# Optimization experiments

Measured on AMD Instinct MI355X. Metric: run time of the kernel, lower is better.

The kernel has to match this reference:

```python
import jax, jax.numpy as jnp
import numpy as np

EMBED_DIM = 768
Q_DIM = 64
V_DIM = 64
WINDOW_SIZE = 3


def setup_inputs() -> dict:
    key = jax.random.key(0)
    ks = jax.random.split(key, 7)
    B, N = 4, 4096
    s = 1.0 / np.sqrt(EMBED_DIM)
    x = jax.random.normal(ks[0], (B, N, EMBED_DIM), dtype=jnp.float32)
    Wq = jax.random.normal(ks[1], (EMBED_DIM, Q_DIM), dtype=jnp.float32) * s
    bq = jax.random.normal(ks[2], (Q_DIM,), dtype=jnp.float32) * 0.01
    Wk = jax.random.normal(ks[3], (EMBED_DIM, Q_DIM), dtype=jnp.float32) * s
    bk = jax.random.normal(ks[4], (Q_DIM,), dtype=jnp.float32) * 0.01
    Wv = jax.random.normal(ks[5], (EMBED_DIM, V_DIM), dtype=jnp.float32) * s
    bv = jax.random.normal(ks[6], (V_DIM,), dtype=jnp.float32) * 0.01
    return {"x": x, "Wq": Wq, "bq": bq, "Wk": Wk, "bk": bk, "Wv": Wv, "bv": bv}


def reference(x, Wq, bq, Wk, bk, Wv, bv):
    # Faithful translation of SliddingWindowAttention.forward, including the
    # original's quirk: diagonal scores are written into columns 0..window_size-1
    # of a full (B, N, N) zero matrix, softmax is taken over ALL N columns
    # (zeros included), and the result is matmul'd with V.
    B, N, _ = x.shape
    Q = x @ Wq + bq  # (B, N, Q_DIM)
    K = x @ Wk + bk  # (B, N, Q_DIM)
    V = x @ Wv + bv  # (B, N, V_DIM)

    half = WINDOW_SIZE // 2
    columns = jnp.zeros((B, N, N), dtype=x.dtype)
    for idx, di in enumerate(range(-half, half + 1)):
        # diagonal offset di: pair row i with column j = i + di (valid rows only)
        rows = np.arange(max(0, -di), N - max(0, di))
        cols_j = rows + di
        c = jnp.einsum('bid,bid->bi', Q[:, rows, :], K[:, cols_j, :])
        columns = columns.at[:, rows, idx].set(c)

    attn = jax.nn.softmax(columns, axis=2)  # (B, N, N)
    return attn @ V  # (B, N, V_DIM)
```

## Files before the change

### kernel.cpp

```cpp
#include <hip/hip_runtime.h>
#include <hip/hip_bf16.h>
#include <math.h>

#define EMBED 768
#define NTOK  4096
#define NB    4
#define ROWS  16384
#define CN    192

typedef __attribute__((ext_vector_type(8))) short bf16x8;
typedef __attribute__((ext_vector_type(8))) unsigned short u16x8;
typedef __attribute__((ext_vector_type(4))) float f32x4;

struct hl16 { unsigned short h, l; };

__device__ inline hl16 split2(float f) {
  hl16 r;
  union { float f; unsigned u; } a; a.f = f;
  unsigned rr = (a.u + 0x7FFFu + ((a.u >> 16) & 1u)) & 0xFFFF0000u;
  r.h = (unsigned short)(rr >> 16);
  union { unsigned u; float f; } hf; hf.u = rr;
  union { float f; unsigned u; } b; b.f = f - hf.f;
  r.l = (unsigned short)((b.u + 0x7FFFu + ((b.u >> 16) & 1u)) >> 16);
  return r;
}

__device__ inline hl16 splitHW(float f) {
  hl16 r;
  __hip_bfloat16 hb = __float2bfloat16(f);
  float hf = __bfloat162float(hb);
  __hip_bfloat16 lb = __float2bfloat16(f - hf);
  r.h = __builtin_bit_cast(unsigned short, hb);
  r.l = __builtin_bit_cast(unsigned short, lb);
  return r;
}

__global__ __launch_bounds__(256) void prep(const float* __restrict__ x,
                                            const float* __restrict__ Wq,
                                            const float* __restrict__ Wk,
                                            const float* __restrict__ Wv,
                                            unsigned short* __restrict__ Wt,
                                            unsigned short* __restrict__ Xt,
                                            float* __restrict__ Vsum) {
  __shared__ float tile[32 * 64];
  const int bid = blockIdx.x;
  const int t   = threadIdx.x;

  if (bid < 6144) {
    const int u   = bid * 4 + (t >> 6);
    const int mt  = u / 24;
    const int ks  = u - mt * 24;
    const int lam = t & 63;
    const int ml  = lam & 15;
    const int q   = lam >> 4;
    const float* src = x + (size_t)(mt * 16 + ml) * EMBED + ks * 32 + q * 8;
    const float4 a0 = *(const float4*)src;
    const float4 a1 = *(const float4*)(src + 4);
    u16x8 hv, lv;
    hl16 s;
    s = splitHW(a0.x); hv[0] = s.h; lv[0] = s.l;
    s = splitHW(a0.y); hv[1] = s.h; lv[1] = s.l;
    s = splitHW(a0.z); hv[2] = s.h; lv[2] = s.l;
    s = splitHW(a0.w); hv[3] = s.h; lv[3] = s.l;
    s = splitHW(a1.x); hv[4] = s.h; lv[4] = s.l;
    s = splitHW(a1.y); hv[5] = s.h; lv[5] = s.l;
    s = splitHW(a1.z); hv[6] = s.h; lv[6] = s.l;
    s = splitHW(a1.w); hv[7] = s.h; lv[7] = s.l;
    unsigned short* dst = Xt + (size_t)(mt * 24 + ks) * 1024 + lam * 8;
    *(u16x8*)dst         = hv;
    *(u16x8*)(dst + 512) = lv;
    return;
  }

  const int b   = bid - 6144;
  const int mat = b / 24;
  const int ks  = b - mat * 24;
  const float* W = (mat == 0) ? Wq : (mat == 1) ? Wk : Wv;

  const float4* src = (const float4*)(W + ks * 2048);
  ((float4*)tile)[t]       = src[t];
  ((float4*)tile)[t + 256] = src[t + 256];
  __syncthreads();

  const int q    = t >> 6;
  const int nloc = t & 63;
  u16x8 hv, lv;
#pragma unroll
  for (int j = 0; j < 8; ++j) {
    hl16 s = split2(tile[(q * 8 + j) * 64 + nloc]);
    hv[j] = s.h; lv[j] = s.l;
  }

  const int n   = mat * 64 + nloc;
  const int nqb = n / 48;
  const int col = n - nqb * 48;
  unsigned short* dst = Wt + (size_t)nqb * 73728 + (size_t)ks * 3072 + q * 384 + col * 8;
  *(u16x8*)dst          = hv;
  *(u16x8*)(dst + 1536) = lv;

  if (b == 0) Vsum[t] = 0.f;
}

__device__ inline void gload_lds16(const unsigned short* g, unsigned short* l) {
  __builtin_amdgcn_global_load_lds(
      (const __attribute__((address_space(1))) unsigned int*)(g),
      (__attribute__((address_space(3))) unsigned int*)(l),
      16, 0, 0);
}

#define MF(A, B, ACC) ACC = __builtin_amdgcn_mfma_f32_16x16x32_bf16(A, B, ACC, 0, 0, 0)

__global__ __launch_bounds__(512, 2) void qkv_mfma(const unsigned short* __restrict__ Xt,
                                                   const unsigned short* __restrict__ Wtu,
                                                   const float* __restrict__ bq,
                                                   const float* __restrict__ bk,
                                                   const float* __restrict__ bv,
                                                   float* __restrict__ C,
                                                   float* __restrict__ Vsum) {
  extern __shared__ unsigned short lds[];

  const int tid  = threadIdx.x;
  const int lane = tid & 63;
  const int wm   = tid >> 6;
  const int nl   = lane & 15;
  const int q    = lane >> 4;
  const int bid  = blockIdx.x;
  const int mc   = (bid & 7) * 8 + (bid >> 5);
  const int nqb  = (bid >> 3) & 3;
  const int nbase = nqb * 48;
  const int r0w  = mc * 256 + wm * 32;
  const int mt0  = mc * 16 + wm * 2;

  {
    const unsigned short* g = Wtu + (size_t)nqb * 73728 + tid * 8;
    unsigned short* l = lds + tid * 8;
#pragma unroll
    for (int i = 0; i < 18; ++i)
      gload_lds16(g + i * 4096, l + i * 4096);
  }

  f32x4 acc00 = {0.f,0.f,0.f,0.f}, acc01 = {0.f,0.f,0.f,0.f}, acc02 = {0.f,0.f,0.f,0.f};
  f32x4 acc10 = {0.f,0.f,0.f,0.f}, acc11 = {0.f,0.f,0.f,0.f}, acc12 = {0.f,0.f,0.f,0.f};

  const bf16x8* XA0 = (const bf16x8*)Xt + (size_t)mt0 * 3072 + lane;
  const bf16x8* XA1 = XA0 + 3072;

  bf16x8 ah0 = XA0[0], al0 = XA0[64];
  bf16x8 ah1 = XA1[0], al1 = XA1[64];

  __syncthreads();

  const bf16x8* LB = (const bf16x8*)lds + q * 48 + nl;

  for (int ks = 0; ks < 24; ++ks) {
    const int o = ks * 384;
    bf16x8 bh0 = LB[o],       bh1 = LB[o + 16],  bh2 = LB[o + 32];
    bf16x8 bl0 = LB[o + 192], bl1 = LB[o + 208], bl2 = LB[o + 224];
    bf16x8 nh0, nl0, nh1, nl1;
    if (ks < 23) {
      nh0 = XA0[(ks + 1) * 128]; nl0 = XA0[(ks + 1) * 128 + 64];
      nh1 = XA1[(ks + 1) * 128]; nl1 = XA1[(ks + 1) * 128 + 64];
    }
    MF(ah0, bh0, acc00); MF(ah1, bh0, acc10);
    MF(ah0, bh1, acc01); MF(ah1, bh1, acc11);
    MF(ah0, bh2, acc02); MF(ah1, bh2, acc12);
    MF(ah0, bl0, acc00); MF(ah1, bl0, acc10);
    MF(ah0, bl1, acc01); MF(ah1, bl1, acc11);
    MF(ah0, bl2, acc02); MF(ah1, bl2, acc12);
    MF(al0, bh0, acc00); MF(al1, bh0, acc10);
    MF(al0, bh1, acc01); MF(al1, bh1, acc11);
    MF(al0, bh2, acc02); MF(al1, bh2, acc12);
    ah0 = nh0; al0 = nl0; ah1 = nh1; al1 = nl1;
  }

#define EPI(MI, NT, ACC) do {                                               \
    const int col = nbase + (NT) * 16 + nl;                                 \
    const float bias = (col < 64) ? bq[col]                                 \
                     : (col < 128) ? bk[col - 64] : bv[col - 128];          \
    const int row = r0w + (MI) * 16 + q * 4;                                \
    C[(size_t)(row + 0) * CN + col] = ACC[0] + bias;                        \
    C[(size_t)(row + 1) * CN + col] = ACC[1] + bias;                        \
    C[(size_t)(row + 2) * CN + col] = ACC[2] + bias;                        \
    C[(size_t)(row + 3) * CN + col] = ACC[3] + bias;                        \
  } while (0)

  EPI(0, 0, acc00); EPI(0, 1, acc01); EPI(0, 2, acc02);
  EPI(1, 0, acc10); EPI(1, 1, acc11); EPI(1, 2, acc12);

#define VS(NT, A0, A1) do {                                                 \
    const int col = nbase + (NT) * 16 + nl;                                 \
    if (col >= 128) {                                                       \
      float s = A0[0] + A0[1] + A0[2] + A0[3]                               \
              + A1[0] + A1[1] + A1[2] + A1[3] + 8.f * bv[col - 128];        \
      s += __shfl_xor(s, 16, 64);                                           \
      s += __shfl_xor(s, 32, 64);                                           \
      if (q == 0) atomicAdd(&Vsum[(r0w >> 12) * 64 + (col - 128)], s);      \
    }                                                                       \
  } while (0)

  VS(0, acc00, acc10); VS(1, acc01, acc11); VS(2, acc02, acc12);
}

__global__ __launch_bounds__(256) void attn_kernel(const float* __restrict__ C,
                                                   const float* __restrict__ Vsum,
                                                   float* __restrict__ out) {
  const int t    = threadIdx.x;
  const int lane = t & 63;
  const int wave = t >> 6;
  const int r = blockIdx.x * 4 + wave;
  const int b = r >> 12;
  const int i = r & (NTOK - 1);

  const float q  = C[(size_t)r * CN + lane];
  const float kc = C[(size_t)r * CN + 64 + lane];
  float km = 0.f, kp = 0.f;
  if (i > 0)        km = C[(size_t)(r - 1) * CN + 64 + lane];
  if (i < NTOK - 1) kp = C[(size_t)(r + 1) * CN + 64 + lane];

  float p0 = q * km, p1 = q * kc, p2 = q * kp;
#pragma unroll
  for (int off = 32; off > 0; off >>= 1) {
    p0 += __shfl_xor(p0, off, 64);
    p1 += __shfl_xor(p1, off, 64);
    p2 += __shfl_xor(p2, off, 64);
  }

  const float s0 = (i > 0) ? p0 : 0.f;
  const float s1 = p1;
  const float s2 = (i < NTOK - 1) ? p2 : 0.f;
  const float m  = fmaxf(fmaxf(s0, s1), fmaxf(s2, 0.f));
  const float e0 = expf(s0 - m);
  const float e1 = expf(s1 - m);
  const float e2 = expf(s2 - m);
  const float ez = expf(-m);
  const float Z  = e0 + e1 + e2 + (float)(NTOK - 3) * ez;

  const size_t vb = ((size_t)b * NTOK) * CN + 128;
  const float v0 = C[vb + lane];
  const float v1 = C[vb + CN + lane];
  const float v2 = C[vb + 2 * (size_t)CN + lane];
  const float vs = Vsum[b * 64 + lane];

  out[(size_t)r * 64 + lane] =
      (e0 * v0 + e1 * v1 + e2 * v2 + ez * (vs - v0 - v1 - v2)) / Z;
}

extern "C" void kernel_launch(void* const* d_in, const int* in_sizes, int n_in,
                              void* d_out, int out_size, void* d_ws, size_t ws_size,
                              hipStream_t stream) {
  const float* x  = (const float*)d_in[0];
  const float* Wq = (const float*)d_in[1];
  const float* bq = (const float*)d_in[2];
  const float* Wk = (const float*)d_in[3];
  const float* bk = (const float*)d_in[4];
  const float* Wv = (const float*)d_in[5];
  const float* bv = (const float*)d_in[6];
  float* out = (float*)d_out;

  float* C    = (float*)d_ws;
  float* Vsum = C + (size_t)ROWS * CN;
  unsigned short* Wt = (unsigned short*)(Vsum + NB * 64);
  unsigned short* Xt = Wt + 4 * 73728;

  prep<<<6216, 256, 0, stream>>>(x, Wq, Wk, Wv, Wt, Xt, Vsum);
  qkv_mfma<<<256, 512, 147456, stream>>>(Xt, Wt, bq, bk, bv, C, Vsum);
  attn_kernel<<<ROWS / 4, 256, 0, stream>>>(C, Vsum, out);
}
```

Before: 127.5 us.

## Split K dimension across two wave groups in QKV MFMA kernel with LDS reduction

Doubles the QKV GEMM block to 1024 threads and splits the 24-step K loop between two groups of eight waves, each handling half of K. The upper group writes its partial accumulators to LDS, which is reused after a barrier, and the lower group adds them before the bias epilogue and the V-sum atomics. This raises the number of waves per block to hide memory latency, since the grid has only 256 blocks. The cost is an extra LDS round trip and two barriers, plus higher register pressure under the 1024-thread launch bound.

Measured after the change: 127.5 us (median of 2 runs). About the same (-0.0%).

```diff
diff --git a/kernel.cpp b/kernel.cpp
--- a/kernel.cpp
+++ b/kernel.cpp
@@ -110,18 +110,20 @@
 
 #define MF(A, B, ACC) ACC = __builtin_amdgcn_mfma_f32_16x16x32_bf16(A, B, ACC, 0, 0, 0)
 
-__global__ __launch_bounds__(512, 2) void qkv_mfma(const unsigned short* __restrict__ Xt,
-                                                   const unsigned short* __restrict__ Wtu,
-                                                   const float* __restrict__ bq,
-                                                   const float* __restrict__ bk,
-                                                   const float* __restrict__ bv,
-                                                   float* __restrict__ C,
-                                                   float* __restrict__ Vsum) {
+__global__ __launch_bounds__(1024, 4) void qkv_mfma(const unsigned short* __restrict__ Xt,
+                                                    const unsigned short* __restrict__ Wtu,
+                                                    const float* __restrict__ bq,
+                                                    const float* __restrict__ bk,
+                                                    const float* __restrict__ bv,
+                                                    float* __restrict__ C,
+                                                    float* __restrict__ Vsum) {
   extern __shared__ unsigned short lds[];
 
   const int tid  = threadIdx.x;
   const int lane = tid & 63;
-  const int wm   = tid >> 6;
+  const int wid  = tid >> 6;
+  const int wm   = wid & 7;
+  const int kh   = wid >> 3;
   const int nl   = lane & 15;
   const int q    = lane >> 4;
   const int bid  = blockIdx.x;
@@ -135,31 +137,31 @@
     const unsigned short* g = Wtu + (size_t)nqb * 73728 + tid * 8;
     unsigned short* l = lds + tid * 8;
 #pragma unroll
-    for (int i = 0; i < 18; ++i)
-      gload_lds16(g + i * 4096, l + i * 4096);
+    for (int i = 0; i < 9; ++i)
+      gload_lds16(g + i * 8192, l + i * 8192);
   }
 
   f32x4 acc00 = {0.f,0.f,0.f,0.f}, acc01 = {0.f,0.f,0.f,0.f}, acc02 = {0.f,0.f,0.f,0.f};
   f32x4 acc10 = {0.f,0.f,0.f,0.f}, acc11 = {0.f,0.f,0.f,0.f}, acc12 = {0.f,0.f,0.f,0.f};
 
-  const bf16x8* XA0 = (const bf16x8*)Xt + (size_t)mt0 * 3072 + lane;
-  const bf16x8* XA1 = XA0 + 3072;
+  const bf16x8* XA0 = (const bf16x8*)Xt + ((size_t)mt0 * 24 + kh * 12) * 128 + lane;
+  const bf16x8* XA1 = XA0 + 24 * 128;
 
   bf16x8 ah0 = XA0[0], al0 = XA0[64];
   bf16x8 ah1 = XA1[0], al1 = XA1[64];
 
   __syncthreads();
 
-  const bf16x8* LB = (const bf16x8*)lds + q * 48 + nl;
-
-  for (int ks = 0; ks < 24; ++ks) {
-    const int o = ks * 384;
+  const bf16x8* LB = (const bf16x8*)lds + kh * 12 * 384 + q * 48 + nl;
+
+  for (int s = 0; s < 12; ++s) {
+    const int o = s * 384;
     bf16x8 bh0 = LB[o],       bh1 = LB[o + 16],  bh2 = LB[o + 32];
     bf16x8 bl0 = LB[o + 192], bl1 = LB[o + 208], bl2 = LB[o + 224];
     bf16x8 nh0, nl0, nh1, nl1;
-    if (ks < 23) {
-      nh0 = XA0[(ks + 1) * 128]; nl0 = XA0[(ks + 1) * 128 + 64];
-      nh1 = XA1[(ks + 1) * 128]; nl1 = XA1[(ks + 1) * 128 + 64];
+    if (s < 11) {
+      nh0 = XA0[(s + 1) * 128]; nl0 = XA0[(s + 1) * 128 + 64];
+      nh1 = XA1[(s + 1) * 128]; nl1 = XA1[(s + 1) * 128 + 64];
     }
     MF(ah0, bh0, acc00); MF(ah1, bh0, acc10);
     MF(ah0, bh1, acc01); MF(ah1, bh1, acc11);
@@ -173,6 +175,37 @@
     ah0 = nh0; al0 = nl0; ah1 = nh1; al1 = nl1;
   }
 
+  float* fl = (float*)lds;
+  __syncthreads();
+
+#define PST(MI, NT, ACC) do {                                               \
+    const int rb = wm * 32 + (MI) * 16 + q * 4;                             \
+    const int c  = (NT) * 16 + nl;                                          \
+    fl[(rb + 0) * 48 + c] = ACC[0];                                         \
+    fl[(rb + 1) * 48 + c] = ACC[1];                                         \
+    fl[(rb + 2) * 48 + c] = ACC[2];                                         \
+    fl[(rb + 3) * 48 + c] = ACC[3];                                         \
+  } while (0)
+
+  if (kh == 1) {
+    PST(0, 0, acc00); PST(0, 1, acc01); PST(0, 2, acc02);
+    PST(1, 0, acc10); PST(1, 1, acc11); PST(1, 2, acc12);
+  }
+  __syncthreads();
+  if (kh == 1) return;
+
+#define ADDP(MI, NT, ACC) do {                                              \
+    const int rb = wm * 32 + (MI) * 16 + q * 4;                             \
+    const int c  = (NT) * 16 + nl;                                          \
+    ACC[0] += fl[(rb + 0) * 48 + c];                                        \
+    ACC[1] += fl[(rb + 1) * 48 + c];                                        \
+    ACC[2] += fl[(rb + 2) * 48 + c];                                        \
+    ACC[3] += fl[(rb + 3) * 48 + c];                                        \
+  } while (0)
+
+  ADDP(0, 0, acc00); ADDP(0, 1, acc01); ADDP(0, 2, acc02);
+  ADDP(1, 0, acc10); ADDP(1, 1, acc11); ADDP(1, 2, acc12);
+
 #define EPI(MI, NT, ACC) do {                                               \
     const int col = nbase + (NT) * 16 + nl;                                 \
     const float bias = (col < 64) ? bq[col]                                 \
@@ -190,11 +223,11 @@
 #define VS(NT, A0, A1) do {                                                 \
     const int col = nbase + (NT) * 16 + nl;                                 \
     if (col >= 128) {                                                       \
-      float s = A0[0] + A0[1] + A0[2] + A0[3]                               \
-              + A1[0] + A1[1] + A1[2] + A1[3] + 8.f * bv[col - 128];        \
-      s += __shfl_xor(s, 16, 64);                                           \
-      s += __shfl_xor(s, 32, 64);                                           \
-      if (q == 0) atomicAdd(&Vsum[(r0w >> 12) * 64 + (col - 128)], s);      \
+      float sv = A0[0] + A0[1] + A0[2] + A0[3]                              \
+               + A1[0] + A1[1] + A1[2] + A1[3] + 8.f * bv[col - 128];       \
+      sv += __shfl_xor(sv, 16, 64);                                         \
+      sv += __shfl_xor(sv, 32, 64);                                         \
+      if (q == 0) atomicAdd(&Vsum[(r0w >> 12) * 64 + (col - 128)], sv);     \
     }                                                                       \
   } while (0)
 
@@ -263,6 +296,6 @@
   unsigned short* Xt = Wt + 4 * 73728;
 
   prep<<<6216, 256, 0, stream>>>(x, Wq, Wk, Wv, Wt, Xt, Vsum);
-  qkv_mfma<<<256, 512, 147456, stream>>>(Xt, Wt, bq, bk, bv, C, Vsum);
+  qkv_mfma<<<256, 1024, 147456, stream>>>(Xt, Wt, bq, bk, bv, C, Vsum);
   attn_kernel<<<ROWS / 4, 256, 0, stream>>>(C, Vsum, out);
 }
```
